# Kernel optimization log

Hardware: AMD Instinct MI355X
Metric: run time of the kernel (lower is better)

Reference implementation:

```python
import jax, jax.numpy as jnp
import numpy as np

B, S, D, H = 2, 2048, 1024, 16
HD = D // H
MAX_BIAS = 8.0


def setup_inputs() -> dict:
    key = jax.random.key(0)
    ks = jax.random.split(key, 5)
    sc = 1.0 / np.sqrt(D)
    return {
        "x": jax.random.normal(ks[0], (B, S, D), jnp.float32),
        "Wq": jax.random.normal(ks[1], (D, D), jnp.float32) * sc,
        "bq": jnp.zeros((D,), jnp.float32),
        "Wk": jax.random.normal(ks[2], (D, D), jnp.float32) * sc,
        "bk": jnp.zeros((D,), jnp.float32),
        "Wv": jax.random.normal(ks[3], (D, D), jnp.float32) * sc,
        "bv": jnp.zeros((D,), jnp.float32),
        "Wo": jax.random.normal(ks[4], (D, D), jnp.float32) * sc,
        "bo": jnp.zeros((D,), jnp.float32),
    }


def _alibi_bias(T, Sk, dtype):
    # slopes: (2 ** (-max_bias / H)) ** (h + 1)
    slopes = (2.0 ** (-MAX_BIAS / H)) ** (jnp.arange(1, H + 1, dtype=dtype))
    qpos = jnp.arange(T)[:, None]
    kpos = jnp.arange(Sk)[None, :]
    rel = -jnp.abs(kpos - qpos).astype(dtype)            # (T, S)
    return slopes[:, None, None] * rel[None]              # (H, T, S)


def reference(x, Wq, bq, Wk, bk, Wv, bv, Wo, bo):
    Bb, Ss, Dd = x.shape
    q = (x @ Wq + bq).reshape(Bb, Ss, H, HD)
    k = (x @ Wk + bk).reshape(Bb, Ss, H, HD)
    v = (x @ Wv + bv).reshape(Bb, Ss, H, HD)
    scores = jnp.einsum("bthd,bshd->bhts", q, k) / jnp.sqrt(jnp.asarray(HD, x.dtype))
    alibi = _alibi_bias(Ss, Ss, x.dtype)                  # (H, T, S)
    causal = jnp.triu(jnp.ones((Ss, Ss), bool), 1)        # key > query -> masked
    scores = scores + alibi[None]
    scores = jnp.where(causal[None, None], -jnp.inf, scores)
    attn = jax.nn.softmax(scores, axis=-1)
    out = jnp.einsum("bhts,bshd->bthd", attn, v).reshape(Bb, Ss, Dd)
    return out @ Wo + bo
```

## Files before the change

kernel.cpp:

```cpp
#include <hip/hip_runtime.h>
#include <hip/hip_bf16.h>

constexpr int B_ = 2, S_ = 2048, D_ = 1024, H_ = 16, HD_ = 64;

typedef __attribute__((ext_vector_type(8))) short bf16x8;
typedef __attribute__((ext_vector_type(4))) short bf16x4;
typedef __attribute__((ext_vector_type(4))) float f32x4;

#if __has_builtin(__builtin_amdgcn_mfma_f32_16x16x16bf16_1k)
#define MFMA16(acc, a, b) \
    (acc) = __builtin_amdgcn_mfma_f32_16x16x16bf16_1k((a), (b), (acc), 0, 0, 0)
#else
#define MFMA16(acc, a, b) \
    asm("v_mfma_f32_16x16x16_bf16 %0, %1, %2, %0" : "+v"(acc) : "v"(a), "v"(b))
#endif

typedef __attribute__((address_space(1))) const unsigned char ga_t;
typedef __attribute__((address_space(3))) unsigned char la_t;
__device__ __forceinline__ void gload_lds16(const void* g, void* l) {
    __builtin_amdgcn_global_load_lds((ga_t*)g, (la_t*)l, 16, 0, 0);
}

__device__ __forceinline__ short f2bf(float x) {
    __hip_bfloat16 h = __float2bfloat16(x);
    return *reinterpret_cast<short*>(&h);
}

__global__ void f32_to_bf16_vec(const float* __restrict__ in,
                                __hip_bfloat16* __restrict__ out, int n) {
    int i = (blockIdx.x * 256 + threadIdx.x) * 4;
    if (i >= n) return;
    float4 v = *reinterpret_cast<const float4*>(in + i);
    union { ushort4 u; __hip_bfloat16 h[4]; } pk;
    pk.h[0] = __float2bfloat16(v.x);
    pk.h[1] = __float2bfloat16(v.y);
    pk.h[2] = __float2bfloat16(v.z);
    pk.h[3] = __float2bfloat16(v.w);
    *reinterpret_cast<ushort4*>(out + i) = pk.u;
}

__global__ void transpose4_f32_to_bf16(const float* __restrict__ w0,
                                       const float* __restrict__ w1,
                                       const float* __restrict__ w2,
                                       const float* __restrict__ w3,
                                       __hip_bfloat16* __restrict__ d0,
                                       __hip_bfloat16* __restrict__ d1,
                                       __hip_bfloat16* __restrict__ d2,
                                       __hip_bfloat16* __restrict__ d3) {
    __shared__ float tile[32][33];
    const int z = blockIdx.z;
    const float* src = z == 0 ? w0 : z == 1 ? w1 : z == 2 ? w2 : w3;
    __hip_bfloat16* dst = z == 0 ? d0 : z == 1 ? d1 : z == 2 ? d2 : d3;
    const int bx = blockIdx.x * 32;
    const int by = blockIdx.y * 32;
    const int c = threadIdx.x & 31;
    const int r0 = threadIdx.x >> 5;
#pragma unroll
    for (int p = 0; p < 4; ++p) {
        int r = r0 + p * 8;
        tile[r][c] = src[(size_t)(by + r) * D_ + bx + c];
    }
    __syncthreads();
#pragma unroll
    for (int p = 0; p < 4; ++p) {
        int r = r0 + p * 8;
        dst[(size_t)(bx + r) * D_ + by + c] = __float2bfloat16(tile[c][r]);
    }
}

__global__ void concat_bias(const float* __restrict__ bq, const float* __restrict__ bk,
                            const float* __restrict__ bv, float* __restrict__ dst) {
    int i = blockIdx.x * 256 + threadIdx.x;
    float v = (i < 1024) ? bq[i] : (i < 2048) ? bk[i - 1024] : bv[i - 2048];
    dst[i] = v;
}

template <bool OUT_F32, int BN_>
__launch_bounds__(256)
__global__ void gemm_bt_kernel(const __hip_bfloat16* __restrict__ A,
                               const __hip_bfloat16* __restrict__ Bt,
                               const float* __restrict__ bias,
                               void* __restrict__ Cout,
                               int M, int N, int K) {
    constexpr int BM = 128, BK = 64;
    constexpr int NI = BN_ / 32;
    __shared__ __hip_bfloat16 As[BM][BK];
    __shared__ __hip_bfloat16 Bs[BN_][BK];

    const int tid = threadIdx.x;
    const int lane = tid & 63;
    const int w = tid >> 6;
    const int wr = w >> 1, wc = w & 1;
    const int g = lane >> 4;
    const int lc = lane & 15;
    const int m0 = blockIdx.x * BM;
    const int n0 = blockIdx.y * BN_;

    const int srow = tid >> 3;
    const int sc0 = (tid & 7) * 8;
    const int scol = sc0 ^ ((srow & 7) << 3);

    f32x4 acc[4][NI] = {};

    for (int k0 = 0; k0 < K; k0 += BK) {
#pragma unroll
        for (int p = 0; p < 4; ++p) {
            int r = p * 32 + srow;
            gload_lds16(&A[(size_t)(m0 + r) * K + k0 + scol], &As[r][sc0]);
        }
#pragma unroll
        for (int p = 0; p < BN_ / 32; ++p) {
            int r = p * 32 + srow;
            gload_lds16(&Bt[(size_t)(n0 + r) * K + k0 + scol], &Bs[r][sc0]);
        }
        __syncthreads();
#pragma unroll
        for (int kk = 0; kk < 2; ++kk) {
            bf16x8 af[4], bfr[NI];
#pragma unroll
            for (int mi = 0; mi < 4; ++mi) {
                int row = wr * 64 + mi * 16 + lc;
                af[mi] = *reinterpret_cast<const bf16x8*>(
                    &As[row][(kk * 32 + g * 8) ^ ((row & 7) << 3)]);
            }
#pragma unroll
            for (int ni = 0; ni < NI; ++ni) {
                int row = wc * (BN_ / 2) + ni * 16 + lc;
                bfr[ni] = *reinterpret_cast<const bf16x8*>(
                    &Bs[row][(kk * 32 + g * 8) ^ ((row & 7) << 3)]);
            }
#pragma unroll
            for (int mi = 0; mi < 4; ++mi)
#pragma unroll
                for (int ni = 0; ni < NI; ++ni)
                    acc[mi][ni] = __builtin_amdgcn_mfma_f32_16x16x32_bf16(af[mi], bfr[ni], acc[mi][ni], 0, 0, 0);
        }
        __syncthreads();
    }

#pragma unroll
    for (int mi = 0; mi < 4; ++mi)
#pragma unroll
        for (int r = 0; r < 4; ++r) {
            int row = m0 + wr * 64 + mi * 16 + g * 4 + r;
#pragma unroll
            for (int ni = 0; ni < NI; ++ni) {
                int col = n0 + wc * (BN_ / 2) + ni * 16 + lc;
                float v = acc[mi][ni][r] + bias[col];
                if (OUT_F32)
                    ((float*)Cout)[(size_t)row * N + col] = v;
                else
                    ((__hip_bfloat16*)Cout)[(size_t)row * N + col] = __float2bfloat16(v);
            }
        }
}

__launch_bounds__(256)
__global__ void attn_kernel(const __hip_bfloat16* __restrict__ qkv,
                            __hip_bfloat16* __restrict__ outb) {
    __shared__ __hip_bfloat16 Ks[2][64][64];
    __shared__ __hip_bfloat16 Vt[2][64][72];

    const int tid = threadIdx.x;
    const int lane = tid & 63;
    const int w = tid >> 6;
    const int bh = blockIdx.x;
    const int b = bh >> 4, h = bh & 15;
    const int g = lane >> 4;
    const int lc = lane & 15;
    const int lq = w * 16 + lc;

    constexpr float LOG2E = 1.44269504088896f;
    constexpr float SC = 0.125f * LOG2E;
    const float slope2 = exp2f(-0.5f * (float)(h + 1)) * LOG2E;

    const size_t rowstride = 3 * D_;
    const size_t base = (size_t)b * S_ * rowstride + h * HD_;

    const int srow = tid >> 3;
    const int sc0 = (tid & 7) * 8;
    const int kscol = sc0 ^ ((srow & 7) << 3);
    const int vwsz = (tid & 7) << 3;

    const int qt = 31 - blockIdx.y;
    const int qg = qt * 64 + lq;

    bf16x8 aq[2];
#pragma unroll
    for (int kk = 0; kk < 2; ++kk)
        aq[kk] = *reinterpret_cast<const bf16x8*>(
            &qkv[base + (size_t)qg * rowstride + kk * 32 + g * 8]);

    float ab[16];
#pragma unroll
    for (int ni = 0; ni < 4; ++ni)
#pragma unroll
        for (int r = 0; r < 4; ++r)
            ab[ni * 4 + r] = slope2 * (float)(16 * ni + 4 * g + r);

    f32x4 o[4] = {};
    float m_run = -3e38f, l_run = 0.f;

#pragma unroll
    for (int p = 0; p < 2; ++p) {
        int r = p * 32 + srow;
        gload_lds16(&qkv[base + (size_t)r * rowstride + D_ + kscol], &Ks[0][r][sc0]);
        uint4 vv = *reinterpret_cast<const uint4*>(
            &qkv[base + (size_t)r * rowstride + 2 * D_ + sc0]);
        const __hip_bfloat16* ve = reinterpret_cast<const __hip_bfloat16*>(&vv);
#pragma unroll
        for (int j = 0; j < 8; ++j)
            Vt[0][sc0 + j][r ^ vwsz] = ve[j];
    }
    __syncthreads();

    int cur = 0;
    for (int kt = 0; kt <= qt; ++kt) {
        const bool havepre = (kt < qt);
        uint4 vpre[2];
        if (havepre) {
#pragma unroll
            for (int p = 0; p < 2; ++p) {
                int r = p * 32 + srow;
                gload_lds16(&qkv[base + (size_t)((kt + 1) * 64 + r) * rowstride + D_ + kscol],
                            &Ks[cur ^ 1][r][sc0]);
                vpre[p] = *reinterpret_cast<const uint4*>(
                    &qkv[base + (size_t)((kt + 1) * 64 + r) * rowstride + 2 * D_ + sc0]);
            }
        }

        f32x4 s[4] = {};
#pragma unroll
        for (int ni = 0; ni < 4; ++ni)
#pragma unroll
            for (int kk = 0; kk < 2; ++kk) {
                int row = ni * 16 + lc;
                bf16x8 kf = *reinterpret_cast<const bf16x8*>(
                    &Ks[cur][row][(kk * 32 + g * 8) ^ ((row & 7) << 3)]);
                s[ni] = __builtin_amdgcn_mfma_f32_16x16x32_bf16(kf, aq[kk], s[ni], 0, 0, 0);
            }

        const bool diag = (kt == qt);
        const float b0 = slope2 * (float)(kt * 64 - qg);
        float v[16];
#pragma unroll
        for (int ni = 0; ni < 4; ++ni)
#pragma unroll
            for (int r = 0; r < 4; ++r) {
                const int koff = 16 * ni + 4 * g + r;
                float t = fmaf(s[ni][r], SC, b0 + ab[ni * 4 + r]);
                if (diag && koff > lq) t = -3e38f;
                v[ni * 4 + r] = t;
            }

        float t8[8], t4[4];
#pragma unroll
        for (int i = 0; i < 8; ++i) t8[i] = fmaxf(v[i], v[i + 8]);
#pragma unroll
        for (int i = 0; i < 4; ++i) t4[i] = fmaxf(t8[i], t8[i + 4]);
        float rm = fmaxf(fmaxf(t4[0], t4[1]), fmaxf(t4[2], t4[3]));
        rm = fmaxf(rm, __shfl_xor(rm, 16, 64));
        rm = fmaxf(rm, __shfl_xor(rm, 32, 64));

        const float mnew = fmaxf(m_run, rm);
        const float alpha = exp2f(m_run - mnew);
        m_run = mnew;

#pragma unroll
        for (int i = 0; i < 16; ++i) v[i] = exp2f(v[i] - mnew);
        float s8[8], s4[4];
#pragma unroll
        for (int i = 0; i < 8; ++i) s8[i] = v[i] + v[i + 8];
#pragma unroll
        for (int i = 0; i < 4; ++i) s4[i] = s8[i] + s8[i + 4];
        float rs = (s4[0] + s4[1]) + (s4[2] + s4[3]);
        rs += __shfl_xor(rs, 16, 64);
        rs += __shfl_xor(rs, 32, 64);
        l_run = l_run * alpha + rs;

        bf16x4 pb[4];
#pragma unroll
        for (int ni = 0; ni < 4; ++ni)
#pragma unroll
            for (int r = 0; r < 4; ++r) {
                o[ni][r] *= alpha;
                pb[ni][r] = f2bf(v[ni * 4 + r]);
            }

#pragma unroll
        for (int oi = 0; oi < 4; ++oi) {
            const int row = oi * 16 + lc;
            const int key = ((row >> 3) & 7) << 3;
#pragma unroll
            for (int ni = 0; ni < 4; ++ni) {
                bf16x4 vf = *reinterpret_cast<const bf16x4*>(
                    &Vt[cur][row][(ni * 16 + 4 * g) ^ key]);
                MFMA16(o[oi], vf, pb[ni]);
            }
        }

        if (havepre) {
#pragma unroll
            for (int p = 0; p < 2; ++p) {
                int r = p * 32 + srow;
                const __hip_bfloat16* ve = reinterpret_cast<const __hip_bfloat16*>(&vpre[p]);
#pragma unroll
                for (int j = 0; j < 8; ++j)
                    Vt[cur ^ 1][sc0 + j][r ^ vwsz] = ve[j];
            }
        }
        __syncthreads();
        cur ^= 1;
    }

    const float inv = 1.0f / l_run;
#pragma unroll
    for (int oi = 0; oi < 4; ++oi) {
        union { ushort4 u; short s[4]; } pk;
#pragma unroll
        for (int r = 0; r < 4; ++r) pk.s[r] = f2bf(o[oi][r] * inv);
        *reinterpret_cast<ushort4*>(
            &outb[(size_t)(b * S_ + qg) * D_ + h * HD_ + oi * 16 + 4 * g]) = pk.u;
    }
}

extern "C" void kernel_launch(void* const* d_in, const int* in_sizes, int n_in,
                              void* d_out, int out_size, void* d_ws, size_t ws_size,
                              hipStream_t stream) {
    const float* x  = (const float*)d_in[0];
    const float* Wq = (const float*)d_in[1];
    const float* bq = (const float*)d_in[2];
    const float* Wk = (const float*)d_in[3];
    const float* bk = (const float*)d_in[4];
    const float* Wv = (const float*)d_in[5];
    const float* bv = (const float*)d_in[6];
    const float* Wo = (const float*)d_in[7];
    const float* bo = (const float*)d_in[8];

    char* ws = (char*)d_ws;
    __hip_bfloat16* xb    = (__hip_bfloat16*)(ws);
    __hip_bfloat16* Wqkvt = (__hip_bfloat16*)(ws + (size_t)(8u  << 20));
    __hip_bfloat16* Wot   = (__hip_bfloat16*)(ws + (size_t)(14u << 20));
    __hip_bfloat16* qkv   = (__hip_bfloat16*)(ws + (size_t)(16u << 20));
    __hip_bfloat16* attnb = (__hip_bfloat16*)(ws + (size_t)(40u << 20));
    float* biasf          = (float*)(ws + (size_t)(48u << 20));

    const int nX = B_ * S_ * D_;

    f32_to_bf16_vec<<<4096, 256, 0, stream>>>(x, xb, nX);
    transpose4_f32_to_bf16<<<dim3(32, 32, 4), 256, 0, stream>>>(
        Wq, Wk, Wv, Wo, Wqkvt, Wqkvt + D_ * D_, Wqkvt + 2 * D_ * D_, Wot);
    concat_bias<<<12, 256, 0, stream>>>(bq, bk, bv, biasf);

    gemm_bt_kernel<false, 128><<<dim3(32, 24), 256, 0, stream>>>(
        xb, Wqkvt, biasf, qkv, B_ * S_, 3 * D_, D_);

    attn_kernel<<<dim3(B_ * H_, S_ / 64), 256, 0, stream>>>(qkv, attnb);

    gemm_bt_kernel<true, 64><<<dim3(32, 16), 256, 0, stream>>>(
        attnb, Wot, bo, (float*)d_out, B_ * S_, D_, D_);
}
```

Measured before the change: 209.5 us.

## Iterate key tiles backward from diagonal and skip online-softmax rescale when max is stable

The attention loop now processes the diagonal key tile first, peeled out with the causal mask, then walks key tiles backward toward the start. Because the ALiBi bias decays with distance, the running max is usually set by the diagonal tile, so later tiles can skip the rescale of the output accumulator and row sum unless some lane sees a larger max (checked with a wave-wide vote). This also removes the per-tile diagonal mask check and folds the bias offset into the max subtraction. It adds a branch and duplicates the tile-processing code.

```diff
diff --git a/kernel.cpp b/kernel.cpp
--- a/kernel.cpp
+++ b/kernel.cpp
@@ -199,14 +199,14 @@
             ab[ni * 4 + r] = slope2 * (float)(16 * ni + 4 * g + r);
 
     f32x4 o[4] = {};
-    float m_run = -3e38f, l_run = 0.f;
 
 #pragma unroll
     for (int p = 0; p < 2; ++p) {
         int r = p * 32 + srow;
-        gload_lds16(&qkv[base + (size_t)r * rowstride + D_ + kscol], &Ks[0][r][sc0]);
+        gload_lds16(&qkv[base + (size_t)(qt * 64 + r) * rowstride + D_ + kscol],
+                    &Ks[0][r][sc0]);
         uint4 vv = *reinterpret_cast<const uint4*>(
-            &qkv[base + (size_t)r * rowstride + 2 * D_ + sc0]);
+            &qkv[base + (size_t)(qt * 64 + r) * rowstride + 2 * D_ + sc0]);
         const __hip_bfloat16* ve = reinterpret_cast<const __hip_bfloat16*>(&vv);
 #pragma unroll
         for (int j = 0; j < 8; ++j)
@@ -214,18 +214,111 @@
     }
     __syncthreads();
 
+    float m_run, l_run;
     int cur = 0;
-    for (int kt = 0; kt <= qt; ++kt) {
-        const bool havepre = (kt < qt);
+    {
+        const bool havepre = (qt > 0);
         uint4 vpre[2];
         if (havepre) {
 #pragma unroll
             for (int p = 0; p < 2; ++p) {
                 int r = p * 32 + srow;
-                gload_lds16(&qkv[base + (size_t)((kt + 1) * 64 + r) * rowstride + D_ + kscol],
+                gload_lds16(&qkv[base + (size_t)((qt - 1) * 64 + r) * rowstride + D_ + kscol],
+                            &Ks[1][r][sc0]);
+                vpre[p] = *reinterpret_cast<const uint4*>(
+                    &qkv[base + (size_t)((qt - 1) * 64 + r) * rowstride + 2 * D_ + sc0]);
+            }
+        }
+
+        f32x4 s[4] = {};
+#pragma unroll
+        for (int ni = 0; ni < 4; ++ni)
+#pragma unroll
+            for (int kk = 0; kk < 2; ++kk) {
+                int row = ni * 16 + lc;
+                bf16x8 kf = *reinterpret_cast<const bf16x8*>(
+                    &Ks[0][row][(kk * 32 + g * 8) ^ ((row & 7) << 3)]);
+                s[ni] = __builtin_amdgcn_mfma_f32_16x16x32_bf16(kf, aq[kk], s[ni], 0, 0, 0);
+            }
+
+        float v[16];
+#pragma unroll
+        for (int ni = 0; ni < 4; ++ni)
+#pragma unroll
+            for (int r = 0; r < 4; ++r) {
+                const int koff = 16 * ni + 4 * g + r;
+                float t = fmaf(s[ni][r], SC, ab[ni * 4 + r]);
+                if (koff > lq) t = -3e38f;
+                v[ni * 4 + r] = t;
+            }
+
+        float t8[8], t4[4];
+#pragma unroll
+        for (int i = 0; i < 8; ++i) t8[i] = fmaxf(v[i], v[i + 8]);
+#pragma unroll
+        for (int i = 0; i < 4; ++i) t4[i] = fmaxf(t8[i], t8[i + 4]);
+        float rm = fmaxf(fmaxf(t4[0], t4[1]), fmaxf(t4[2], t4[3]));
+        rm = fmaxf(rm, __shfl_xor(rm, 16, 64));
+        rm = fmaxf(rm, __shfl_xor(rm, 32, 64));
+
+        m_run = rm - slope2 * (float)lq;
+
+#pragma unroll
+        for (int i = 0; i < 16; ++i) v[i] = exp2f(v[i] - rm);
+        float s8[8], s4[4];
+#pragma unroll
+        for (int i = 0; i < 8; ++i) s8[i] = v[i] + v[i + 8];
+#pragma unroll
+        for (int i = 0; i < 4; ++i) s4[i] = s8[i] + s8[i + 4];
+        float rs = (s4[0] + s4[1]) + (s4[2] + s4[3]);
+        rs += __shfl_xor(rs, 16, 64);
+        rs += __shfl_xor(rs, 32, 64);
+        l_run = rs;
+
+        bf16x4 pb[4];
+#pragma unroll
+        for (int ni = 0; ni < 4; ++ni)
+#pragma unroll
+            for (int r = 0; r < 4; ++r)
+                pb[ni][r] = f2bf(v[ni * 4 + r]);
+
+#pragma unroll
+        for (int oi = 0; oi < 4; ++oi) {
+            const int row = oi * 16 + lc;
+            const int key = ((row >> 3) & 7) << 3;
+#pragma unroll
+            for (int ni = 0; ni < 4; ++ni) {
+                bf16x4 vf = *reinterpret_cast<const bf16x4*>(
+                    &Vt[0][row][(ni * 16 + 4 * g) ^ key]);
+                MFMA16(o[oi], vf, pb[ni]);
+            }
+        }
+
+        if (havepre) {
+#pragma unroll
+            for (int p = 0; p < 2; ++p) {
+                int r = p * 32 + srow;
+                const __hip_bfloat16* ve = reinterpret_cast<const __hip_bfloat16*>(&vpre[p]);
+#pragma unroll
+                for (int j = 0; j < 8; ++j)
+                    Vt[1][sc0 + j][r ^ vwsz] = ve[j];
+            }
+        }
+        __syncthreads();
+        cur = 1;
+    }
+
+    for (int kt = qt - 1; kt >= 0; --kt) {
+        const bool havepre = (kt > 0);
+        uint4 vpre[2];
+        if (havepre) {
+#pragma unroll
+            for (int p = 0; p < 2; ++p) {
+                int r = p * 32 + srow;
+                gload_lds16(&qkv[base + (size_t)((kt - 1) * 64 + r) * rowstride + D_ + kscol],
                             &Ks[cur ^ 1][r][sc0]);
                 vpre[p] = *reinterpret_cast<const uint4*>(
-                    &qkv[base + (size_t)((kt + 1) * 64 + r) * rowstride + 2 * D_ + sc0]);
+                    &qkv[base + (size_t)((kt - 1) * 64 + r) * rowstride + 2 * D_ + sc0]);
             }
         }
 
@@ -240,18 +333,12 @@
                 s[ni] = __builtin_amdgcn_mfma_f32_16x16x32_bf16(kf, aq[kk], s[ni], 0, 0, 0);
             }
 
-        const bool diag = (kt == qt);
-        const float b0 = slope2 * (float)(kt * 64 - qg);
         float v[16];
 #pragma unroll
         for (int ni = 0; ni < 4; ++ni)
 #pragma unroll
-            for (int r = 0; r < 4; ++r) {
-                const int koff = 16 * ni + 4 * g + r;
-                float t = fmaf(s[ni][r], SC, b0 + ab[ni * 4 + r]);
-                if (diag && koff > lq) t = -3e38f;
-                v[ni * 4 + r] = t;
-            }
+            for (int r = 0; r < 4; ++r)
+                v[ni * 4 + r] = fmaf(s[ni][r], SC, ab[ni * 4 + r]);
 
         float t8[8], t4[4];
 #pragma unroll
@@ -262,12 +349,22 @@
         rm = fmaxf(rm, __shfl_xor(rm, 16, 64));
         rm = fmaxf(rm, __shfl_xor(rm, 32, 64));
 
-        const float mnew = fmaxf(m_run, rm);
-        const float alpha = exp2f(m_run - mnew);
-        m_run = mnew;
-
-#pragma unroll
-        for (int i = 0; i < 16; ++i) v[i] = exp2f(v[i] - mnew);
+        const float b0 = slope2 * (float)(kt * 64 - qg);
+        float mloc = m_run - b0;
+        if (__any(rm > mloc)) {
+            const float mnew = fmaxf(m_run, rm + b0);
+            const float alpha = exp2f(m_run - mnew);
+#pragma unroll
+            for (int oi = 0; oi < 4; ++oi)
+#pragma unroll
+                for (int r = 0; r < 4; ++r) o[oi][r] *= alpha;
+            l_run *= alpha;
+            m_run = mnew;
+            mloc = m_run - b0;
+        }
+
+#pragma unroll
+        for (int i = 0; i < 16; ++i) v[i] = exp2f(v[i] - mloc);
         float s8[8], s4[4];
 #pragma unroll
         for (int i = 0; i < 8; ++i) s8[i] = v[i] + v[i + 8];
@@ -276,16 +373,14 @@
         float rs = (s4[0] + s4[1]) + (s4[2] + s4[3]);
         rs += __shfl_xor(rs, 16, 64);
         rs += __shfl_xor(rs, 32, 64);
-        l_run = l_run * alpha + rs;
+        l_run += rs;
 
         bf16x4 pb[4];
 #pragma unroll
         for (int ni = 0; ni < 4; ++ni)
 #pragma unroll
-            for (int r = 0; r < 4; ++r) {
-                o[ni][r] *= alpha;
+            for (int r = 0; r < 4; ++r)
                 pb[ni][r] = f2bf(v[ni * 4 + r]);
-            }
 
 #pragma unroll
         for (int oi = 0; oi < 4; ++oi) {
```

Measured after the change: 194.1 us. -7.4%, faster.
